# Kernel optimization log

Hardware: AMD Instinct MI355X
Metric: run time of the kernel (lower is better)

Reference implementation:

```python
import jax, jax.numpy as jnp
import numpy as np

B, T, F = 128, 512, 16   # batch, seq len, n_features
K, PAD, H = 5, 2, 32     # conv kernel, padding, per-feature GRU hidden
NEG = 0.01               # LeakyReLU default negative slope


def setup_inputs() -> dict:
    key = jax.random.key(0)
    ks = iter(jax.random.split(key, 64))

    def u(shape, fan):
        s = 1.0 / np.sqrt(fan)
        return jax.random.uniform(next(ks), shape, jnp.float32, -s, s)

    inp = {}
    inp['x'] = jax.random.normal(next(ks), (B, 2, T), jnp.float32)
    # gru_enc: input=2, hidden=F, unidirectional (torch layout: W_ih [3H,I], W_hh [3H,H])
    inp['enc_Wih'] = u((3 * F, 2), F)
    inp['enc_Whh'] = u((3 * F, F), F)
    inp['enc_bih'] = u((3 * F,), F)
    inp['enc_bhh'] = u((3 * F,), F)
    # last_layers_gru (per feature): input=1, hidden=H, bidirectional
    for d in ('f', 'b'):
        inp[f'g1_Wih_{d}'] = u((F, 3 * H, 1), H)
        inp[f'g1_Whh_{d}'] = u((F, 3 * H, H), H)
        inp[f'g1_bih_{d}'] = u((F, 3 * H), H)
        inp[f'g1_bhh_{d}'] = u((F, 3 * H), H)
    # layers_gru (per feature): input=2H, hidden=H, unidirectional
    inp['g2_Wih'] = u((F, 3 * H, 2 * H), H)
    inp['g2_Whh'] = u((F, 3 * H, H), H)
    inp['g2_bih'] = u((F, 3 * H), H)
    inp['g2_bhh'] = u((F, 3 * H), H)
    # ConvTranspose1d weights, torch layout [C_in, C_out, K]
    inp['w3'] = u((F, 32, 64, K), 32 * K)
    inp['b3'] = u((F, 64), 32 * K)
    inp['w2'] = u((F, 64, 128, K), 64 * K)
    inp['b2'] = u((F, 128), 64 * K)
    inp['w1'] = u((F, 128, 1, K), 128 * K)
    inp['b1'] = u((F, 1), 128 * K)
    return inp


def gru(x, Wih, Whh, bih, bhh):
    # x: [B, T, I] -> [B, T, H]; torch GRU cell math
    Hh = Whh.shape[1]
    xp = jnp.einsum('bti,gi->btg', x, Wih) + bih  # [B,T,3H], input proj for all t

    def step(h, xt):
        g = h @ Whh.T + bhh
        xr, xz, xn = jnp.split(xt, 3, -1)
        hr, hz, hn = jnp.split(g, 3, -1)
        r = jax.nn.sigmoid(xr + hr)
        z = jax.nn.sigmoid(xz + hz)
        n = jnp.tanh(xn + r * hn)
        h = (1 - z) * n + z * h
        return h, h

    h0 = jnp.zeros((x.shape[0], Hh), x.dtype)
    _, ys = jax.lax.scan(step, h0, jnp.swapaxes(xp, 0, 1))
    return jnp.swapaxes(ys, 0, 1)


def bigru(x, Wf, Hf, bif, bhf, Wb, Hb, bib, bhb):
    fwd = gru(x, Wf, Hf, bif, bhf)
    bwd = gru(x[:, ::-1], Wb, Hb, bib, bhb)[:, ::-1]
    return jnp.concatenate([fwd, bwd], -1)


def convT(x, w, b):
    # ConvTranspose1d(stride=1, padding=PAD): x [B,Cin,T], w [Cin,Cout,K]
    wc = jnp.flip(w, -1).transpose(1, 0, 2)  # -> [Cout,Cin,K] cross-correlation kernel
    y = jax.lax.conv_general_dilated(
        x, wc, (1,), [(K - 1 - PAD, K - 1 - PAD)],
        dimension_numbers=('NCH', 'OIH', 'NCH'))
    return y + b[None, :, None]


def reference(x, enc_Wih, enc_Whh, enc_bih, enc_bhh,
              g1_Wih_f, g1_Whh_f, g1_bih_f, g1_bhh_f,
              g1_Wih_b, g1_Whh_b, g1_bih_b, g1_bhh_b,
              g2_Wih, g2_Whh, g2_bih, g2_bhh,
              w3, b3, w2, b2, w1, b1):
    leaky = lambda v: jnp.where(v >= 0, v, NEG * v)
    # encoder GRU over time: x [B,2,T] -> [B,T,F]
    h = gru(jnp.swapaxes(x, 1, 2), enc_Wih, enc_Whh, enc_bih, enc_bhh)

    def per_feature(xi, W1f, H1f, bi1f, bh1f, W1b, H1b, bi1b, bh1b,
                    W2, H2, bi2, bh2, w3_, b3_, w2_, b2_, w1_, b1_):
        # xi: [B,T] single feature channel
        u = bigru(xi[..., None], W1f, H1f, bi1f, bh1f, W1b, H1b, bi1b, bh1b)  # [B,T,2H]
        u = gru(u, W2, H2, bi2, bh2)        # [B,T,H]
        u = jnp.swapaxes(u, 1, 2)           # [B,H,T]
        u = leaky(convT(u, w3_, b3_))       # [B,64,T]
        u = leaky(convT(u, w2_, b2_))       # [B,128,T]
        u = leaky(convT(u, w1_, b1_))       # [B,1,T]
        return u[:, 0]                      # [B,T]

    feats = jnp.moveaxis(h, 2, 0)           # [F,B,T]
    out = jax.vmap(per_feature)(feats,
                                g1_Wih_f, g1_Whh_f, g1_bih_f, g1_bhh_f,
                                g1_Wih_b, g1_Whh_b, g1_bih_b, g1_bhh_b,
                                g2_Wih, g2_Whh, g2_bih, g2_bhh,
                                w3, b3, w2, b2, w1, b1)  # [F,B,T]
    return jnp.moveaxis(out, 0, 2)          # [B,T,F]
```

## Files before the change

### kernel.cpp

```cpp
#include <hip/hip_runtime.h>
#include <math.h>

#define BB 128
#define TT 512
#define FF 16

typedef _Float16 half8 __attribute__((ext_vector_type(8)));
typedef float floatx4 __attribute__((ext_vector_type(4)));

union HU { uint4 u; half8 h; };

__device__ __forceinline__ float bf2f(unsigned short u){
  union { unsigned int i; float f; } c; c.i = ((unsigned int)u) << 16; return c.f;
}
__device__ __forceinline__ unsigned short f2bf(float f){
  union { float f; unsigned int i; } c; c.f = f;
  unsigned int x = c.i;
  unsigned int r = (x + 0x7fffu + ((x >> 16) & 1u)) >> 16;
  return (unsigned short)r;
}
__device__ __forceinline__ float sigm(float x){
  return __builtin_amdgcn_rcpf(1.f + __expf(-x));
}
__device__ __forceinline__ float tanh_fast(float x){
  x = fminf(15.f, fmaxf(-15.f, x));
  float e = __expf(-2.f*x);
  return (1.f - e)*__builtin_amdgcn_rcpf(1.f + e);
}
__device__ __forceinline__ float lrelu(float v){ return v >= 0.f ? v : 0.01f*v; }

__device__ __forceinline__ unsigned int packhl(float v){
  _Float16 hh = (_Float16)v;
  float hf = (float)hh;
  _Float16 hl = (_Float16)(v - hf);
  union { _Float16 h; unsigned short s; } a, b;
  a.h = hh; b.h = hl;
  return (unsigned int)a.s | ((unsigned int)b.s << 16);
}

__device__ __forceinline__ void unpackAB(uint4 P0, uint4 P1, HU& Ah, HU& Al){
  Ah.u.x = (P0.x & 0xffffu) | (P0.y << 16);
  Ah.u.y = (P0.z & 0xffffu) | (P0.w << 16);
  Ah.u.z = (P1.x & 0xffffu) | (P1.y << 16);
  Ah.u.w = (P1.z & 0xffffu) | (P1.w << 16);
  Al.u.x = (P0.x >> 16) | (P0.y & 0xffff0000u);
  Al.u.y = (P0.z >> 16) | (P0.w & 0xffff0000u);
  Al.u.z = (P1.x >> 16) | (P1.y & 0xffff0000u);
  Al.u.w = (P1.z >> 16) | (P1.w & 0xffff0000u);
}

#define MFMA16(A,B,C) __builtin_amdgcn_mfma_f32_16x16x32_f16((A),(B),(C),0,0,0)

__global__ __launch_bounds__(256) void fill_kernel(unsigned short* out, int n, float v){
  int i = blockIdx.x*256 + threadIdx.x;
  if (i < n) out[i] = f2bf(v);
}

__global__ __launch_bounds__(256) void detect1_kernel(const unsigned short* x, float* maxbuf){
  __shared__ float red[256];
  const int base = blockIdx.x*4096 + threadIdx.x*16;
  const uint4* p = (const uint4*)(x + base);
  uint4 a = p[0], b = p[1];
  unsigned int ws[8] = {a.x,a.y,a.z,a.w,b.x,b.y,b.z,b.w};
  float m = 0.f;
  #pragma unroll
  for (int i=0;i<8;i++){
    float v0 = fabsf(bf2f((unsigned short)(ws[i] & 0xffffu)));
    float v1 = fabsf(bf2f((unsigned short)(ws[i] >> 16)));
    if (!isfinite(v0)) v0 = 3e38f;
    if (!isfinite(v1)) v1 = 3e38f;
    m = fmaxf(m, fmaxf(v0, v1));
  }
  red[threadIdx.x] = m; __syncthreads();
  for (int s=128; s>0; s>>=1){
    if (threadIdx.x < s) red[threadIdx.x] = fmaxf(red[threadIdx.x], red[threadIdx.x+s]);
    __syncthreads();
  }
  if (threadIdx.x == 0) maxbuf[blockIdx.x] = red[0];
}
__global__ __launch_bounds__(64) void detect2_kernel(const float* maxbuf, int* flag){
  if (threadIdx.x == 0){
    float m = 0.f;
    for (int i=0;i<32;i++) m = fmaxf(m, maxbuf[i]);
    *flag = (m < 1e4f) ? 1 : 0;
  }
}

struct CvtArgs { const void* p[23]; int sz[23]; int ofs[23]; };

__global__ __launch_bounds__(256) void convert_kernel(CvtArgs a, const int* flag, float* dst){
  const int i = blockIdx.x;
  const int n = a.sz[i];
  const int start = blockIdx.y * 16384;
  if (start >= n) return;
  const int end = (start + 16384 < n) ? start + 16384 : n;
  float* d = dst + a.ofs[i];
  const int s4 = start >> 2, e4 = end >> 2;
  if (*flag){
    const unsigned short* s = (const unsigned short*)a.p[i];
    for (int e = s4 + threadIdx.x; e < e4; e += 256){
      uint2 w = *(const uint2*)(s + 4*e);
      float4 o;
      o.x = bf2f((unsigned short)(w.x & 0xffffu));
      o.y = bf2f((unsigned short)(w.x >> 16));
      o.z = bf2f((unsigned short)(w.y & 0xffffu));
      o.w = bf2f((unsigned short)(w.y >> 16));
      *(float4*)(d + 4*e) = o;
    }
  } else {
    const float* s = (const float*)a.p[i];
    for (int e = s4 + threadIdx.x; e < e4; e += 256)
      *(float4*)(d + 4*e) = *(const float4*)(s + 4*e);
  }
}

__global__ __launch_bounds__(256) void prep16_kernel(
    const float* __restrict__ cvt, _Float16* __restrict__ h16,
    int o6, int o10, int o14, int o13, int o17, int o19, int o2)
{
  const int i = blockIdx.x*256 + threadIdx.x;
  const int y = blockIdx.y;
  if (y == 0){ if (i < 49152) h16[i]          = (_Float16)cvt[o6  + i]; }
  else if (y == 1){ if (i < 49152) h16[49152 + i]  = (_Float16)cvt[o10 + i]; }
  else if (y == 2){ if (i < 49152) h16[98304 + i]  = (_Float16)cvt[o14 + i]; }
  else if (y == 3){ if (i < 98304) h16[147456 + i] = (_Float16)cvt[o13 + i]; }
  else if (y == 4){
    if (i < 163840){
      int ci = i & 31, co = (i >> 5) & 63, fj = i >> 11;
      int f = fj / 5, j = fj - 5*f;
      h16[245760 + i] = (_Float16)cvt[o17 + ((f*32 + ci)*64 + co)*5 + j];
    }
  } else if (y == 5){
    if (i < 655360){
      int ci = i & 63, co = (i >> 6) & 127, fj = i >> 13;
      int f = fj / 5, j = fj - 5*f;
      h16[409600 + i] = (_Float16)cvt[o19 + ((f*64 + ci)*128 + co)*5 + j];
    }
  } else {
    if (i < 1536){
      int k = i & 31, row = i >> 5;
      h16[1064960 + i] = (k < 16) ? (_Float16)cvt[o2 + row*16 + k] : (_Float16)0.f;
    }
  }
}

__global__ __launch_bounds__(128) void xt_kernel(const float* __restrict__ cvt, float* __restrict__ xTp){
  const int t = blockIdx.x, b = threadIdx.x;
  xTp[t*BB + b]            = cvt[(b*2 + 0)*TT + t];
  xTp[65536 + t*BB + b]    = cvt[(b*2 + 1)*TT + t];
}

__global__ __launch_bounds__(64) void enc_kernel(
    const float* __restrict__ xTp, const _Float16* __restrict__ whhE,
    const float* __restrict__ Wih, const float* __restrict__ bih,
    const float* __restrict__ bhh, float* __restrict__ xfeatT)
{
  const int b0 = blockIdx.x*16;
  const int l = threadIdx.x, ml = l & 15, q = l >> 4;
  __shared__ unsigned int Hpk[2][16][20];
  half8 Bw[3];
  #pragma unroll
  for (int c=0;c<3;c++)
    Bw[c] = *(const half8*)(whhE + (16*c + ml)*32 + 8*q);
  float w0r=Wih[ml*2],      w1r=Wih[ml*2+1],      bir=bih[ml],    bhr=bhh[ml];
  float w0z=Wih[(16+ml)*2], w1z=Wih[(16+ml)*2+1], biz=bih[16+ml], bhz=bhh[16+ml];
  float w0n=Wih[(32+ml)*2], w1n=Wih[(32+ml)*2+1], bin_=bih[32+ml], bhn=bhh[32+ml];
  float hm[4] = {0,0,0,0};
  HU Ah, Al; Ah.u = make_uint4(0,0,0,0); Al.u = Ah.u;
  const floatx4 z4 = {0.f,0.f,0.f,0.f};
  int pp = 0;
  floatx4 x0v = *(const floatx4*)(xTp + b0 + 4*q);
  floatx4 x1v = *(const floatx4*)(xTp + 65536 + b0 + 4*q);
  for (int t=0;t<TT;t++){
    const int tn = (t < 511) ? t+1 : t;
    floatx4 x0n = *(const floatx4*)(xTp + tn*BB + b0 + 4*q);
    floatx4 x1n = *(const floatx4*)(xTp + 65536 + tn*BB + b0 + 4*q);
    floatx4 C[3];
    #pragma unroll
    for (int c=0;c<3;c++){
      C[c] = MFMA16(Al.h, Bw[c], z4);
      C[c] = MFMA16(Ah.h, Bw[c], C[c]);
    }
    #pragma unroll
    for (int r=0;r<4;r++){
      float xb0 = x0v[r], xb1 = x1v[r];
      float rr = sigm(fmaf(w0r,xb0,fmaf(w1r,xb1,bir)) + C[0][r] + bhr);
      float zz = sigm(fmaf(w0z,xb0,fmaf(w1z,xb1,biz)) + C[1][r] + bhz);
      float nn = tanh_fast(fmaf(w0n,xb0,fmaf(w1n,xb1,bin_)) + rr*(C[2][r] + bhn));
      float hn = nn + zz*(hm[r] - nn);
      hm[r] = hn;
      Hpk[pp][4*q + r][ml] = packhl(hn);
      xfeatT[((size_t)ml*TT + t)*BB + b0 + 4*q + r] = hn;
    }
    __syncthreads();
    if (q < 2){
      uint4 P0 = *(const uint4*)&Hpk[pp][ml][8*q];
      uint4 P1 = *(const uint4*)&Hpk[pp][ml][8*q + 4];
      unpackAB(P0, P1, Ah, Al);
    } else { Ah.u = make_uint4(0,0,0,0); Al.u = Ah.u; }
    pp ^= 1;
    x0v = x0n; x1v = x1n;
  }
}

__global__ __launch_bounds__(128) void g1b_kernel(
    const float* __restrict__ xT, const _Float16* __restrict__ whh_h,
    const float* __restrict__ wih, const float* __restrict__ bih,
    const float* __restrict__ bhh, _Float16* __restrict__ trace)
{
  const int f = blockIdx.x, b0 = blockIdx.y*16;
  const int wid = threadIdx.x >> 6, l = threadIdx.x & 63, ml = l & 15, q = l >> 4;
  __shared__ unsigned int Hpk[2][16][36];
  half8 Bw[3];
  #pragma unroll
  for (int i=0;i<3;i++){
    int tc = 2*i + wid;
    Bw[i] = *(const half8*)(whh_h + (size_t)f*3072 + (16*tc + ml)*32 + 8*q);
  }
  const int j = 16*wid + ml, base = f*96;
  float wir=wih[base+j], wiz=wih[base+32+j], win=wih[base+64+j];
  float br_=bih[base+j]+bhh[base+j];
  float bz_=bih[base+32+j]+bhh[base+32+j];
  float bin_=bih[base+64+j], bhn_=bhh[base+64+j];
  float hm[4] = {0,0,0,0};
  HU Ah, Al; Ah.u = make_uint4(0,0,0,0); Al.u = Ah.u;
  const floatx4 z4 = {0.f,0.f,0.f,0.f};
  int pp = 0;
  floatx4 xv = *(const floatx4*)(xT + ((size_t)f*TT + 511)*BB + b0 + 4*q);
  const int dostore = (wid == (q >> 1));
  for (int s=0;s<512;s++){
    const int t = 511 - s;
    const int tn = (s < 511) ? t-1 : t;
    floatx4 xnx = *(const floatx4*)(xT + ((size_t)f*TT + tn)*BB + b0 + 4*q);
    floatx4 C[3];
    #pragma unroll
    for (int i=0;i<3;i++){
      C[i] = MFMA16(Al.h, Bw[i], z4);
      C[i] = MFMA16(Ah.h, Bw[i], C[i]);
    }
    #pragma unroll
    for (int r=0;r<4;r++){
      float xb = xv[r];
      float rr = sigm(fmaf(wir, xb, br_) + C[0][r]);
      float zz = sigm(fmaf(wiz, xb, bz_) + C[1][r]);
      float nn = tanh_fast(fmaf(win, xb, bin_) + rr*(C[2][r] + bhn_));
      float hn = nn + zz*(hm[r] - nn);
      hm[r] = hn;
      Hpk[pp][4*q + r][j] = packhl(hn);
    }
    __syncthreads();
    {
      uint4 P0 = *(const uint4*)&Hpk[pp][ml][8*q];
      uint4 P1 = *(const uint4*)&Hpk[pp][ml][8*q + 4];
      unpackAB(P0, P1, Ah, Al);
    }
    if (dostore)
      *(uint4*)(trace + (((size_t)(f*BB + b0 + ml))*TT + t)*32 + 8*q) = Ah.u;
    pp ^= 1;
    xv = xnx;
  }
}

__global__ __launch_bounds__(128) void g2_kernel(
    const float* __restrict__ xT,
    const _Float16* __restrict__ wh1_h, const float* __restrict__ wih1,
    const float* __restrict__ bih1, const float* __restrict__ bhh1,
    const _Float16* __restrict__ wh2_h, const _Float16* __restrict__ w2i_h,
    const float* __restrict__ bih2, const float* __restrict__ bhh2,
    _Float16* __restrict__ trace)
{
  const int f = blockIdx.x, b0 = blockIdx.y*16;
  const int wid = threadIdx.x >> 6, l = threadIdx.x & 63, ml = l & 15, q = l >> 4;
  __shared__ unsigned int Hpk1[2][16][36];
  __shared__ unsigned int Hpk2[2][16][36];
  half8 B1[3], Bh2[3], Bx0[3], Bx1[3];
  #pragma unroll
  for (int i=0;i<3;i++){
    int tc = 2*i + wid;
    B1[i]  = *(const half8*)(wh1_h + (size_t)f*3072 + (16*tc + ml)*32 + 8*q);
    Bh2[i] = *(const half8*)(wh2_h + (size_t)f*3072 + (16*tc + ml)*32 + 8*q);
    Bx0[i] = *(const half8*)(w2i_h + (size_t)f*6144 + (16*tc + ml)*64 + 8*q);
    Bx1[i] = *(const half8*)(w2i_h + (size_t)f*6144 + (16*tc + ml)*64 + 32 + 8*q);
  }
  const int j = 16*wid + ml, base = f*96;
  float wir=wih1[base+j], wiz=wih1[base+32+j], win=wih1[base+64+j];
  float br1_=bih1[base+j]+bhh1[base+j];
  float bz1_=bih1[base+32+j]+bhh1[base+32+j];
  float bin1_=bih1[base+64+j], bhn1_=bhh1[base+64+j];
  float br2_=bih2[base+j]+bhh2[base+j];
  float bz2_=bih2[base+32+j]+bhh2[base+32+j];
  float bin2_=bih2[base+64+j], bhn2_=bhh2[base+64+j];
  float h1[4] = {0,0,0,0};
  float h2[4] = {0,0,0,0};
  HU A1h, A1l, A2h, A2l;
  A1h.u = make_uint4(0,0,0,0); A1l.u = A1h.u; A2h.u = A1h.u; A2l.u = A1h.u;
  const floatx4 z4 = {0.f,0.f,0.f,0.f};
  const size_t rowb = ((size_t)(f*BB + b0 + ml))*TT;
  const int dostore = (wid == (q >> 1));

  {
    floatx4 x0v = *(const floatx4*)(xT + (size_t)f*TT*BB + b0 + 4*q);
    #pragma unroll
    for (int r=0;r<4;r++){
      float xb = x0v[r];
      float rr = sigm(fmaf(wir, xb, br1_));
      float zz = sigm(fmaf(wiz, xb, bz1_));
      float nn = tanh_fast(fmaf(win, xb, bin1_) + rr*bhn1_);
      float hn = (1.f - zz)*nn;
      h1[r] = hn;
      Hpk1[0][4*q + r][j] = packhl(hn);
    }
    __syncthreads();
    uint4 P0 = *(const uint4*)&Hpk1[0][ml][8*q];
    uint4 P1 = *(const uint4*)&Hpk1[0][ml][8*q + 4];
    unpackAB(P0, P1, A1h, A1l);
  }
  int pp = 1;
  uint4 Ub = *(const uint4*)(trace + (rowb + 0)*32 + 8*q);
  floatx4 xv = *(const floatx4*)(xT + ((size_t)f*TT + 1)*BB + b0 + 4*q);
  for (int t=0;t<512;t++){
    const int tn1 = (t < 511) ? t+1 : t;
    const int tn2 = (t < 510) ? t+2 : 511;
    uint4 Ubn = *(const uint4*)(trace + (rowb + tn1)*32 + 8*q);
    floatx4 xnx = *(const floatx4*)(xT + ((size_t)f*TT + tn2)*BB + b0 + 4*q);
    floatx4 C1[3];
    #pragma unroll
    for (int i=0;i<3;i++){
      C1[i] = MFMA16(A1l.h, B1[i], z4);
      C1[i] = MFMA16(A1h.h, B1[i], C1[i]);
    }
    HU Abw; Abw.u = Ub;
    floatx4 Cr, Cz, Cnh, Cnx;
    Cr = MFMA16(A2l.h, Bh2[0], z4); Cr = MFMA16(A2h.h, Bh2[0], Cr);
    Cr = MFMA16(A1l.h, Bx0[0], Cr); Cr = MFMA16(A1h.h, Bx0[0], Cr);
    Cr = MFMA16(Abw.h, Bx1[0], Cr);
    Cz = MFMA16(A2l.h, Bh2[1], z4); Cz = MFMA16(A2h.h, Bh2[1], Cz);
    Cz = MFMA16(A1l.h, Bx0[1], Cz); Cz = MFMA16(A1h.h, Bx0[1], Cz);
    Cz = MFMA16(Abw.h, Bx1[1], Cz);
    Cnh = MFMA16(A2l.h, Bh2[2], z4); Cnh = MFMA16(A2h.h, Bh2[2], Cnh);
    Cnx = MFMA16(A1l.h, Bx0[2], z4); Cnx = MFMA16(A1h.h, Bx0[2], Cnx);
    Cnx = MFMA16(Abw.h, Bx1[2], Cnx);
    #pragma unroll
    for (int r=0;r<4;r++){
      float xb = xv[r];
      float rr1 = sigm(fmaf(wir, xb, br1_) + C1[0][r]);
      float zz1 = sigm(fmaf(wiz, xb, bz1_) + C1[1][r]);
      float nn1 = tanh_fast(fmaf(win, xb, bin1_) + rr1*(C1[2][r] + bhn1_));
      float hn1 = nn1 + zz1*(h1[r] - nn1);
      h1[r] = hn1;
      Hpk1[pp][4*q + r][j] = packhl(hn1);

      float rr2 = sigm(Cr[r] + br2_);
      float zz2 = sigm(Cz[r] + bz2_);
      float nn2 = tanh_fast(Cnx[r] + bin2_ + rr2*(Cnh[r] + bhn2_));
      float hn2 = nn2 + zz2*(h2[r] - nn2);
      h2[r] = hn2;
      Hpk2[pp][4*q + r][j] = packhl(hn2);
    }
    __syncthreads();
    {
      uint4 P0 = *(const uint4*)&Hpk1[pp][ml][8*q];
      uint4 P1 = *(const uint4*)&Hpk1[pp][ml][8*q + 4];
      unpackAB(P0, P1, A1h, A1l);
      uint4 Q0 = *(const uint4*)&Hpk2[pp][ml][8*q];
      uint4 Q1 = *(const uint4*)&Hpk2[pp][ml][8*q + 4];
      unpackAB(Q0, Q1, A2h, A2l);
    }
    if (dostore)
      *(uint4*)(trace + (rowb + t)*32 + 8*q) = A2h.u;
    Ub = Ubn; xv = xnx; pp ^= 1;
  }
}

#define UTP 40
#define C3P 72
#define C2P 136
__global__ __launch_bounds__(256) void conv_kernel(
    const _Float16* __restrict__ u2,
    const _Float16* __restrict__ w3T, const float* __restrict__ b3,
    const _Float16* __restrict__ w2T, const float* __restrict__ b2,
    const float* __restrict__ w1, const float* __restrict__ b1,
    void* __restrict__ outv, const int* __restrict__ flag)
{
  const int t0 = blockIdx.x * 32;
  const int b  = blockIdx.y;
  const int f  = blockIdx.z;
  const int tid = threadIdx.x;
  const int w = tid >> 6, l = tid & 63, ml = l & 15, q = l >> 4;

  __shared__ __align__(16) _Float16 utb[52][UTP];
  __shared__ __align__(16) _Float16 c3T[52][C3P];
  __shared__ __align__(16) _Float16 c2T[36][C2P];
  __shared__ float red[8][32];

  const _Float16* urow = u2 + ((size_t)(f*BB + b)*TT)*32;
  const floatx4 z4 = {0.f,0.f,0.f,0.f};

  for (int k = tid; k < 52*4; k += 256){
    int n = k >> 2, seg = k & 3;
    int tg = t0 - 6 + n;
    uint4 v = make_uint4(0,0,0,0);
    if (n < 44 && tg >= 0 && tg < TT) v = *(const uint4*)(urow + (size_t)tg*32 + seg*8);
    *(uint4*)&utb[n][seg*8] = v;
  }
  for (int k = tid; k < 96; k += 256){
    int rr = 40 + (k >> 3), seg = k & 7;
    *(uint4*)&c3T[rr][seg*8] = make_uint4(0,0,0,0);
  }
  __syncthreads();

  {
    half8 A3[5];
    #pragma unroll
    for (int jj=0;jj<5;jj++)
      A3[jj] = *(const half8*)(w3T + (((size_t)f*5 + jj)*64 + 16*w + ml)*32 + 8*q);
    float bv[4];
    #pragma unroll
    for (int r=0;r<4;r++) bv[r] = b3[f*64 + 16*w + 4*q + r];
    #pragma unroll
    for (int nt=0;nt<3;nt++){
      floatx4 acc = z4;
      #pragma unroll
      for (int jj=0;jj<5;jj++){
        half8 Bb = *(const half8*)&utb[16*nt + ml + 4 - jj][8*q];
        acc = MFMA16(A3[jj], Bb, acc);
      }
      int tm = 16*nt + ml;
      if (tm < 40){
        int G = t0 - 4 + tm;
        unsigned int pk[2];
        #pragma unroll
        for (int h=0;h<2;h++){
          float v0 = acc[2*h]   + bv[2*h];   v0 = lrelu(v0);
          float v1 = acc[2*h+1] + bv[2*h+1]; v1 = lrelu(v1);
          if (G < 0 || G >= TT){ v0 = 0.f; v1 = 0.f; }
          union { _Float16 hh; unsigned short s; } c0, c1;
          c0.hh = (_Float16)v0; c1.hh = (_Float16)v1;
          pk[h] = (unsigned int)c0.s | ((unsigned int)c1.s << 16);
        }
        *(uint2*)&c3T[tm][16*w + 4*q] = make_uint2(pk[0], pk[1]);
      }
    }
  }
  __syncthreads();

  {
    half8 A2f[5][2][2];
    #pragma unroll
    for (int jj=0;jj<5;jj++)
      #pragma unroll
      for (int ch=0;ch<2;ch++)
        #pragma unroll
        for (int mi=0;mi<2;mi++)
          A2f[jj][ch][mi] = *(const half8*)(w2T + (((size_t)f*5 + jj)*128 + 16*(2*w+mi) + ml)*64 + 32*ch + 8*q);
    float bv2[2][4];
    #pragma unroll
    for (int mi=0;mi<2;mi++)
      #pragma unroll
      for (int r=0;r<4;r++) bv2[mi][r] = b2[f*128 + 16*(2*w+mi) + 4*q + r];
    #pragma unroll
    for (int nt=0;nt<3;nt++){
      floatx4 a0 = z4, a1 = z4;
      #pragma unroll
      for (int jj=0;jj<5;jj++){
        #pragma unroll
        for (int ch=0;ch<2;ch++){
          half8 Bb = *(const half8*)&c3T[16*nt + ml + 4 - jj][32*ch + 8*q];
          a0 = MFMA16(A2f[jj][ch][0], Bb, a0);
          a1 = MFMA16(A2f[jj][ch][1], Bb, a1);
        }
      }
      int p = 16*nt + ml;
      if (p < 36){
        int G = t0 - 2 + p;
        #pragma unroll
        for (int mi=0;mi<2;mi++){
          unsigned int pk[2];
          #pragma unroll
          for (int h=0;h<2;h++){
            float v0 = (mi ? a1[2*h]   : a0[2*h])   + bv2[mi][2*h];   v0 = lrelu(v0);
            float v1 = (mi ? a1[2*h+1] : a0[2*h+1]) + bv2[mi][2*h+1]; v1 = lrelu(v1);
            if (G < 0 || G >= TT){ v0 = 0.f; v1 = 0.f; }
            union { _Float16 hh; unsigned short s; } c0, c1;
            c0.hh = (_Float16)v0; c1.hh = (_Float16)v1;
            pk[h] = (unsigned int)c0.s | ((unsigned int)c1.s << 16);
          }
          *(uint2*)&c2T[p][16*(2*w+mi) + 4*q] = make_uint2(pk[0], pk[1]);
        }
      }
    }
  }
  __syncthreads();

  {
    const int tl = tid & 31, cg = tid >> 5;
    const float* wp = w1 + ((size_t)f*128 + cg*16)*5;
    float acc = 0.f;
    #pragma unroll
    for (int jj=0;jj<5;jj++){
      int row = tl + 4 - jj;
      union { uint4 u; _Float16 h[8]; } u0, u1;
      u0.u = *(const uint4*)&c2T[row][cg*16];
      u1.u = *(const uint4*)&c2T[row][cg*16 + 8];
      #pragma unroll
      for (int i=0;i<8;i++){
        acc = fmaf(wp[i*5 + jj],     (float)u0.h[i], acc);
        acc = fmaf(wp[(8+i)*5 + jj], (float)u1.h[i], acc);
      }
    }
    red[cg][tl] = acc;
  }
  __syncthreads();
  if (tid < 32){
    float s = b1[f];
    #pragma unroll
    for (int cg=0;cg<8;cg++) s += red[cg][tid];
    s = lrelu(s);
    size_t oi = ((size_t)b*TT + t0 + tid)*FF + f;
    if (*flag) ((unsigned short*)outv)[oi] = f2bf(s);
    else       ((float*)outv)[oi] = s;
  }
}

extern "C" void kernel_launch(void* const* d_in, const int* in_sizes, int n_in,
                              void* d_out, int out_size, void* d_ws, size_t ws_size,
                              hipStream_t stream)
{
  static const int esz[23] = {
    131072,
    96, 768, 48, 48,
    1536, 49152, 1536, 1536,
    1536, 49152, 1536, 1536,
    98304, 49152, 1536, 1536,
    163840, 1024,
    655360, 2048,
    10240, 16
  };
  const size_t NEED = (size_t)16*1024*1024 + (size_t)64*1024*1024;

  float diag = 0.f;
  if (n_in != 23) diag = 2000.f + n_in;
  else {
    for (int i=0;i<23;i++) if (in_sizes[i] != esz[i]) { diag = 1000.f + i; break; }
    if (diag == 0.f && ws_size < NEED) diag = 500.f + (float)(ws_size >> 20);
  }
  if (diag != 0.f){
    hipLaunchKernelGGL(fill_kernel, dim3((out_size+255)/256), dim3(256), 0, stream,
                       (unsigned short*)d_out, out_size, diag);
    return;
  }

  float* cvt = (float*)d_ws;
  int* flagp = (int*)((char*)d_ws + (5ull<<20));
  float* maxbuf = (float*)((char*)d_ws + (5ull<<20) + 256);
  _Float16* h16 = (_Float16*)((char*)d_ws + (6ull<<20));
  float* xTp = (float*)((char*)d_ws + (9ull<<20));
  float* xfeatT = (float*)((char*)d_ws + (10ull<<20));
  _Float16* trace = (_Float16*)((char*)d_ws + (14ull<<20));

  CvtArgs a;
  int ofs = 0;
  for (int i=0;i<23;i++){ a.p[i] = d_in[i]; a.sz[i] = esz[i]; a.ofs[i] = ofs; ofs += esz[i]; }
  const float* c[23];
  for (int i=0;i<23;i++) c[i] = cvt + a.ofs[i];

  hipLaunchKernelGGL(detect1_kernel, dim3(32), dim3(256), 0, stream,
                     (const unsigned short*)d_in[0], maxbuf);
  hipLaunchKernelGGL(detect2_kernel, dim3(1), dim3(64), 0, stream, maxbuf, flagp);
  hipLaunchKernelGGL(convert_kernel, dim3(23, 40), dim3(256), 0, stream, a, flagp, cvt);
  hipLaunchKernelGGL(prep16_kernel, dim3(2560, 7), dim3(256), 0, stream,
                     cvt, h16, a.ofs[6], a.ofs[10], a.ofs[14], a.ofs[13],
                     a.ofs[17], a.ofs[19], a.ofs[2]);
  hipLaunchKernelGGL(xt_kernel, dim3(TT), dim3(BB), 0, stream, cvt, xTp);
  hipLaunchKernelGGL(enc_kernel, dim3(BB/16), dim3(64), 0, stream,
                     xTp, h16 + 1064960, c[1], c[3], c[4], xfeatT);
  hipLaunchKernelGGL(g1b_kernel, dim3(FF, 8), dim3(128), 0, stream,
                     xfeatT, h16 + 49152, c[9], c[11], c[12], trace);
  hipLaunchKernelGGL(g2_kernel, dim3(FF, 8), dim3(128), 0, stream,
                     xfeatT, h16 + 0, c[5], c[7], c[8],
                     h16 + 98304, h16 + 147456, c[15], c[16], trace);
  hipLaunchKernelGGL(conv_kernel, dim3(TT/32, BB, FF), dim3(256), 0, stream,
                     trace, h16 + 245760, c[18], h16 + 409600, c[20], c[21], c[22],
                     d_out, flagp);
}
```

Measured before the change: 1.554 ms.

## Run forward and backward GRU1 in parallel and widen conv time tiles

After: 1.339 ms. -13.8%, faster.

```diff
diff --git a/kernel.cpp b/kernel.cpp
--- a/kernel.cpp
+++ b/kernel.cpp
@@ -261,6 +261,74 @@
   }
 }
 
+__global__ __launch_bounds__(128) void g1bf_kernel(
+    const float* __restrict__ xT,
+    const _Float16* __restrict__ whhB_h, const float* __restrict__ wihB,
+    const float* __restrict__ bihB, const float* __restrict__ bhhB,
+    const _Float16* __restrict__ whhF_h, const float* __restrict__ wihF,
+    const float* __restrict__ bihF, const float* __restrict__ bhhF,
+    _Float16* __restrict__ traceB, _Float16* __restrict__ traceF)
+{
+  const int f = blockIdx.x, b0 = blockIdx.y*16, dir = blockIdx.z;
+  const _Float16* whh_h = dir ? whhF_h : whhB_h;
+  const float* wih = dir ? wihF : wihB;
+  const float* bih = dir ? bihF : bihB;
+  const float* bhh = dir ? bhhF : bhhB;
+  _Float16* trace = dir ? traceF : traceB;
+  const int wid = threadIdx.x >> 6, l = threadIdx.x & 63, ml = l & 15, q = l >> 4;
+  __shared__ unsigned int Hpk[2][16][36];
+  half8 Bw[3];
+  #pragma unroll
+  for (int i=0;i<3;i++){
+    int tc = 2*i + wid;
+    Bw[i] = *(const half8*)(whh_h + (size_t)f*3072 + (16*tc + ml)*32 + 8*q);
+  }
+  const int j = 16*wid + ml, base = f*96;
+  float wir=wih[base+j], wiz=wih[base+32+j], win=wih[base+64+j];
+  float br_=bih[base+j]+bhh[base+j];
+  float bz_=bih[base+32+j]+bhh[base+32+j];
+  float bin_=bih[base+64+j], bhn_=bhh[base+64+j];
+  float hm[4] = {0,0,0,0};
+  HU Ah, Al; Ah.u = make_uint4(0,0,0,0); Al.u = Ah.u;
+  const floatx4 z4 = {0.f,0.f,0.f,0.f};
+  int pp = 0;
+  const int tfirst = dir ? 0 : 511;
+  floatx4 xv = *(const floatx4*)(xT + ((size_t)f*TT + tfirst)*BB + b0 + 4*q);
+  const int dostore = (wid == (q >> 1));
+  for (int s=0;s<512;s++){
+    const int t  = dir ? s : 511 - s;
+    const int sn = (s < 511) ? s+1 : s;
+    const int tn = dir ? sn : 511 - sn;
+    floatx4 xnx = *(const floatx4*)(xT + ((size_t)f*TT + tn)*BB + b0 + 4*q);
+    floatx4 C[3];
+    #pragma unroll
+    for (int i=0;i<3;i++){
+      C[i] = MFMA16(Al.h, Bw[i], z4);
+      C[i] = MFMA16(Ah.h, Bw[i], C[i]);
+    }
+    #pragma unroll
+    for (int r=0;r<4;r++){
+      float xb = xv[r];
+      float rr = sigm(fmaf(wir, xb, br_) + C[0][r]);
+      float zz = sigm(fmaf(wiz, xb, bz_) + C[1][r]);
+      float nn = tanh_fast(fmaf(win, xb, bin_) + rr*(C[2][r] + bhn_));
+      float hn = nn + zz*(hm[r] - nn);
+      hm[r] = hn;
+      Hpk[pp][4*q + r][j] = packhl(hn);
+    }
+    __syncthreads();
+    {
+      uint4 P0 = *(const uint4*)&Hpk[pp][ml][8*q];
+      uint4 P1 = *(const uint4*)&Hpk[pp][ml][8*q + 4];
+      unpackAB(P0, P1, Ah, Al);
+    }
+    if (dostore)
+      *(uint4*)(trace + (((size_t)(f*BB + b0 + ml))*TT + t)*32 + 8*q) = Ah.u;
+    pp ^= 1;
+    xv = xnx;
+  }
+}
+
 __global__ __launch_bounds__(128) void g2_kernel(
     const float* __restrict__ xT,
     const _Float16* __restrict__ wh1_h, const float* __restrict__ wih1,
@@ -372,6 +440,68 @@
   }
 }
 
+__global__ __launch_bounds__(128) void g2f_kernel(
+    const _Float16* __restrict__ wh2_h, const _Float16* __restrict__ w2i_h,
+    const float* __restrict__ bih2, const float* __restrict__ bhh2,
+    const _Float16* __restrict__ traceF, _Float16* __restrict__ traceB)
+{
+  const int f = blockIdx.x, b0 = blockIdx.y*16;
+  const int wid = threadIdx.x >> 6, l = threadIdx.x & 63, ml = l & 15, q = l >> 4;
+  __shared__ unsigned int Hpk2[2][16][36];
+  half8 Bh2[3], Bx0[3], Bx1[3];
+  #pragma unroll
+  for (int i=0;i<3;i++){
+    int tc = 2*i + wid;
+    Bh2[i] = *(const half8*)(wh2_h + (size_t)f*3072 + (16*tc + ml)*32 + 8*q);
+    Bx0[i] = *(const half8*)(w2i_h + (size_t)f*6144 + (16*tc + ml)*64 + 8*q);
+    Bx1[i] = *(const half8*)(w2i_h + (size_t)f*6144 + (16*tc + ml)*64 + 32 + 8*q);
+  }
+  const int j = 16*wid + ml, base = f*96;
+  float br2_=bih2[base+j]+bhh2[base+j];
+  float bz2_=bih2[base+32+j]+bhh2[base+32+j];
+  float bin2_=bih2[base+64+j], bhn2_=bhh2[base+64+j];
+  float h2[4] = {0,0,0,0};
+  HU A2h, A2l; A2h.u = make_uint4(0,0,0,0); A2l.u = A2h.u;
+  const floatx4 z4 = {0.f,0.f,0.f,0.f};
+  const size_t rowb = ((size_t)(f*BB + b0 + ml))*TT;
+  const int dostore = (wid == (q >> 1));
+  int pp = 0;
+  uint4 UbF = *(const uint4*)(traceF + (rowb + 0)*32 + 8*q);
+  uint4 UbB = *(const uint4*)(traceB + (rowb + 0)*32 + 8*q);
+  for (int t=0;t<512;t++){
+    const int tn = (t < 511) ? t+1 : t;
+    uint4 UbFn = *(const uint4*)(traceF + (rowb + tn)*32 + 8*q);
+    uint4 UbBn = *(const uint4*)(traceB + (rowb + tn)*32 + 8*q);
+    HU AF; AF.u = UbF;
+    HU AB; AB.u = UbB;
+    floatx4 Cr, Cz, Cnh, Cnx;
+    Cr = MFMA16(A2l.h, Bh2[0], z4); Cr = MFMA16(A2h.h, Bh2[0], Cr);
+    Cr = MFMA16(AF.h, Bx0[0], Cr);  Cr = MFMA16(AB.h, Bx1[0], Cr);
+    Cz = MFMA16(A2l.h, Bh2[1], z4); Cz = MFMA16(A2h.h, Bh2[1], Cz);
+    Cz = MFMA16(AF.h, Bx0[1], Cz);  Cz = MFMA16(AB.h, Bx1[1], Cz);
+    Cnh = MFMA16(A2l.h, Bh2[2], z4); Cnh = MFMA16(A2h.h, Bh2[2], Cnh);
+    Cnx = MFMA16(AF.h, Bx0[2], z4);  Cnx = MFMA16(AB.h, Bx1[2], Cnx);
+    #pragma unroll
+    for (int r=0;r<4;r++){
+      float rr2 = sigm(Cr[r] + br2_);
+      float zz2 = sigm(Cz[r] + bz2_);
+      float nn2 = tanh_fast(Cnx[r] + bin2_ + rr2*(Cnh[r] + bhn2_));
+      float hn2 = nn2 + zz2*(h2[r] - nn2);
+      h2[r] = hn2;
+      Hpk2[pp][4*q + r][j] = packhl(hn2);
+    }
+    __syncthreads();
+    {
+      uint4 Q0 = *(const uint4*)&Hpk2[pp][ml][8*q];
+      uint4 Q1 = *(const uint4*)&Hpk2[pp][ml][8*q + 4];
+      unpackAB(Q0, Q1, A2h, A2l);
+    }
+    if (dostore)
+      *(uint4*)(traceB + (rowb + t)*32 + 8*q) = A2h.u;
+    UbF = UbFn; UbB = UbBn; pp ^= 1;
+  }
+}
+
 #define UTP 40
 #define C3P 72
 #define C2P 136
@@ -382,30 +512,26 @@
     const float* __restrict__ w1, const float* __restrict__ b1,
     void* __restrict__ outv, const int* __restrict__ flag)
 {
-  const int t0 = blockIdx.x * 32;
+  const int t0 = blockIdx.x * 64;
   const int b  = blockIdx.y;
   const int f  = blockIdx.z;
   const int tid = threadIdx.x;
   const int w = tid >> 6, l = tid & 63, ml = l & 15, q = l >> 4;
 
-  __shared__ __align__(16) _Float16 utb[52][UTP];
-  __shared__ __align__(16) _Float16 c3T[52][C3P];
-  __shared__ __align__(16) _Float16 c2T[36][C2P];
-  __shared__ float red[8][32];
+  __shared__ __align__(16) _Float16 utb[84][UTP];
+  __shared__ __align__(16) _Float16 c3T[84][C3P];
+  __shared__ __align__(16) _Float16 c2T[68][C2P];
+  __shared__ float red[4][64];
 
   const _Float16* urow = u2 + ((size_t)(f*BB + b)*TT)*32;
   const floatx4 z4 = {0.f,0.f,0.f,0.f};
 
-  for (int k = tid; k < 52*4; k += 256){
+  for (int k = tid; k < 76*4; k += 256){
     int n = k >> 2, seg = k & 3;
     int tg = t0 - 6 + n;
     uint4 v = make_uint4(0,0,0,0);
-    if (n < 44 && tg >= 0 && tg < TT) v = *(const uint4*)(urow + (size_t)tg*32 + seg*8);
+    if (tg >= 0 && tg < TT) v = *(const uint4*)(urow + (size_t)tg*32 + seg*8);
     *(uint4*)&utb[n][seg*8] = v;
-  }
-  for (int k = tid; k < 96; k += 256){
-    int rr = 40 + (k >> 3), seg = k & 7;
-    *(uint4*)&c3T[rr][seg*8] = make_uint4(0,0,0,0);
   }
   __syncthreads();
 
@@ -418,7 +544,7 @@
     #pragma unroll
     for (int r=0;r<4;r++) bv[r] = b3[f*64 + 16*w + 4*q + r];
     #pragma unroll
-    for (int nt=0;nt<3;nt++){
+    for (int nt=0;nt<5;nt++){
       floatx4 acc = z4;
       #pragma unroll
       for (int jj=0;jj<5;jj++){
@@ -426,7 +552,7 @@
         acc = MFMA16(A3[jj], Bb, acc);
       }
       int tm = 16*nt + ml;
-      if (tm < 40){
+      if (tm < 72){
         int G = t0 - 4 + tm;
         unsigned int pk[2];
         #pragma unroll
@@ -459,7 +585,7 @@
       #pragma unroll
       for (int r=0;r<4;r++) bv2[mi][r] = b2[f*128 + 16*(2*w+mi) + 4*q + r];
     #pragma unroll
-    for (int nt=0;nt<3;nt++){
+    for (int nt=0;nt<5;nt++){
       floatx4 a0 = z4, a1 = z4;
       #pragma unroll
       for (int jj=0;jj<5;jj++){
@@ -471,7 +597,7 @@
         }
       }
       int p = 16*nt + ml;
-      if (p < 36){
+      if (p < 68){
         int G = t0 - 2 + p;
         #pragma unroll
         for (int mi=0;mi<2;mi++){
@@ -493,28 +619,30 @@
   __syncthreads();
 
   {
-    const int tl = tid & 31, cg = tid >> 5;
-    const float* wp = w1 + ((size_t)f*128 + cg*16)*5;
+    const int tl = tid & 63, cg = tid >> 6;
+    const float* wp = w1 + ((size_t)f*128 + cg*32)*5;
     float acc = 0.f;
     #pragma unroll
     for (int jj=0;jj<5;jj++){
       int row = tl + 4 - jj;
-      union { uint4 u; _Float16 h[8]; } u0, u1;
-      u0.u = *(const uint4*)&c2T[row][cg*16];
-      u1.u = *(const uint4*)&c2T[row][cg*16 + 8];
+      union { uint4 u; _Float16 h[8]; } u0, u1, u2_, u3;
+      u0.u  = *(const uint4*)&c2T[row][cg*32];
+      u1.u  = *(const uint4*)&c2T[row][cg*32 + 8];
+      u2_.u = *(const uint4*)&c2T[row][cg*32 + 16];
+      u3.u  = *(const uint4*)&c2T[row][cg*32 + 24];
       #pragma unroll
       for (int i=0;i<8;i++){
-        acc = fmaf(wp[i*5 + jj],     (float)u0.h[i], acc);
-        acc = fmaf(wp[(8+i)*5 + jj], (float)u1.h[i], acc);
+        acc = fmaf(wp[i*5 + jj],      (float)u0.h[i],  acc);
+        acc = fmaf(wp[(8+i)*5 + jj],  (float)u1.h[i],  acc);
+        acc = fmaf(wp[(16+i)*5 + jj], (float)u2_.h[i], acc);
+        acc = fmaf(wp[(24+i)*5 + jj], (float)u3.h[i],  acc);
       }
     }
     red[cg][tl] = acc;
   }
   __syncthreads();
-  if (tid < 32){
-    float s = b1[f];
-    #pragma unroll
-    for (int cg=0;cg<8;cg++) s += red[cg][tid];
+  if (tid < 64){
+    float s = b1[f] + red[0][tid] + red[1][tid] + red[2][tid] + red[3][tid];
     s = lrelu(s);
     size_t oi = ((size_t)b*TT + t0 + tid)*FF + f;
     if (*flag) ((unsigned short*)outv)[oi] = f2bf(s);
@@ -557,6 +685,8 @@
   float* xTp = (float*)((char*)d_ws + (9ull<<20));
   float* xfeatT = (float*)((char*)d_ws + (10ull<<20));
   _Float16* trace = (_Float16*)((char*)d_ws + (14ull<<20));
+  _Float16* traceF = (_Float16*)((char*)d_ws + (80ull<<20));
+  const bool bigws = (ws_size >= (145ull<<20));
 
   CvtArgs a;
   int ofs = 0;
@@ -574,12 +704,23 @@
   hipLaunchKernelGGL(xt_kernel, dim3(TT), dim3(BB), 0, stream, cvt, xTp);
   hipLaunchKernelGGL(enc_kernel, dim3(BB/16), dim3(64), 0, stream,
                      xTp, h16 + 1064960, c[1], c[3], c[4], xfeatT);
-  hipLaunchKernelGGL(g1b_kernel, dim3(FF, 8), dim3(128), 0, stream,
-                     xfeatT, h16 + 49152, c[9], c[11], c[12], trace);
-  hipLaunchKernelGGL(g2_kernel, dim3(FF, 8), dim3(128), 0, stream,
-                     xfeatT, h16 + 0, c[5], c[7], c[8],
-                     h16 + 98304, h16 + 147456, c[15], c[16], trace);
-  hipLaunchKernelGGL(conv_kernel, dim3(TT/32, BB, FF), dim3(256), 0, stream,
+  if (bigws){
+    hipLaunchKernelGGL(g1bf_kernel, dim3(FF, 8, 2), dim3(128), 0, stream,
+                       xfeatT,
+                       h16 + 49152, c[9], c[11], c[12],
+                       h16 + 0,     c[5], c[7],  c[8],
+                       trace, traceF);
+    hipLaunchKernelGGL(g2f_kernel, dim3(FF, 8), dim3(128), 0, stream,
+                       h16 + 98304, h16 + 147456, c[15], c[16],
+                       traceF, trace);
+  } else {
+    hipLaunchKernelGGL(g1b_kernel, dim3(FF, 8), dim3(128), 0, stream,
+                       xfeatT, h16 + 49152, c[9], c[11], c[12], trace);
+    hipLaunchKernelGGL(g2_kernel, dim3(FF, 8), dim3(128), 0, stream,
+                       xfeatT, h16 + 0, c[5], c[7], c[8],
+                       h16 + 98304, h16 + 147456, c[15], c[16], trace);
+  }
+  hipLaunchKernelGGL(conv_kernel, dim3(TT/64, BB, FF), dim3(256), 0, stream,
                      trace, h16 + 245760, c[18], h16 + 409600, c[20], c[21], c[22],
                      d_out, flagp);
 }
```
